# Optimization experiments

Measured on AMD Instinct MI355X. Metric: run time of the kernel, lower is better.

## Reference

```python
import jax, jax.numpy as jnp
import numpy as np

# OmniNet(deepqmc) reconstruction: ElectronicSchNet v1 (2 interactions, kernel_dim=8,
# embedding_dim=16, dist_feat_dim=4) + Linear(16,1,bias=False) orbital + sum over electrons.
# SchNet v1: shared w and g per interaction, spin-dependent h (same/anti), nuclear
# messages via learned nuclear embeddings Y. Subnets: w = 2-layer log-DNN 4->6->8 with SSP,
# h = Linear(16,8), g = Linear(8,16). SSP(x) = softplus(x) - log(2).

N_UP, N_DOWN = 16, 16
N_ELEC = N_UP + N_DOWN
N_ATOMS = 8
DIST_FEAT, KERNEL, EMBED = 4, 8, 16
N_INTER = 2
BATCH = 4096


def ssp(x):
    return jax.nn.softplus(x) - jnp.log(2.0).astype(x.dtype)


def setup_inputs() -> dict:
    key = jax.random.key(0)
    ks = jax.random.split(key, 16)
    s = 0.5  # init scale
    return {
        'dists_nuc': jax.random.uniform(ks[0], (BATCH, N_ELEC, N_ATOMS, DIST_FEAT), jnp.float32),
        'dists_elec': jax.random.uniform(ks[1], (BATCH, N_ELEC, N_ELEC, DIST_FEAT), jnp.float32),
        'X': jax.random.normal(ks[2], (1, EMBED), jnp.float32) * s,          # electron embedding (n_up==n_down)
        'Y': jax.random.normal(ks[3], (N_ATOMS, KERNEL), jnp.float32) * s,   # nuclear embeddings
        'w1': jax.random.normal(ks[4], (N_INTER, DIST_FEAT, 6), jnp.float32) * s,
        'wb1': jax.random.normal(ks[5], (N_INTER, 6), jnp.float32) * s,
        'w2': jax.random.normal(ks[6], (N_INTER, 6, KERNEL), jnp.float32) * s,
        'wb2': jax.random.normal(ks[7], (N_INTER, KERNEL), jnp.float32) * s,
        'hs_w': jax.random.normal(ks[8], (N_INTER, EMBED, KERNEL), jnp.float32) * s,
        'hs_b': jax.random.normal(ks[9], (N_INTER, KERNEL), jnp.float32) * s,
        'ha_w': jax.random.normal(ks[10], (N_INTER, EMBED, KERNEL), jnp.float32) * s,
        'ha_b': jax.random.normal(ks[11], (N_INTER, KERNEL), jnp.float32) * s,
        'g_w': jax.random.normal(ks[12], (N_INTER, KERNEL, EMBED), jnp.float32) * s,
        'g_b': jax.random.normal(ks[13], (N_INTER, EMBED), jnp.float32) * s,
        'orb_w': jax.random.normal(ks[14], (EMBED,), jnp.float32) * s,
    }


def reference(dists_nuc, dists_elec, X, Y, w1, wb1, w2, wb2, hs_w, hs_b, ha_w, ha_b, g_w, g_b, orb_w):
    B, n_elec = dists_elec.shape[:2]
    dt = dists_elec.dtype
    spins = jnp.concatenate([jnp.zeros(N_UP, jnp.int32), jnp.ones(N_DOWN, jnp.int32)])
    eye = jnp.eye(n_elec, dtype=bool)
    same = ((spins[:, None] == spins[None, :]) & ~eye).astype(dt)  # (i,j) same-spin, no self
    anti = (spins[:, None] != spins[None, :]).astype(dt)

    # initial embeddings: all electrons share X[0] since n_up == n_down
    x = jnp.broadcast_to(X[0], (B, n_elec, EMBED))

    for n in range(N_INTER):
        def w_net(e):  # (..., 4) -> (..., 8)
            return ssp(e @ w1[n] + wb1[n]) @ w2[n] + wb2[n]
        we = w_net(dists_elec)            # (B, i, j, K)
        wn = w_net(dists_nuc)             # (B, i, M, K)
        hs = x @ hs_w[n] + hs_b[n]        # (B, j, K) same-spin message features
        ha = x @ ha_w[n] + ha_b[n]        # (B, j, K) anti-spin
        z = (jnp.einsum('bijk,ij,bjk->bik', we, same, hs)
             + jnp.einsum('bijk,ij,bjk->bik', we, anti, ha)
             + jnp.einsum('bimk,mk->bik', wn, Y))
        x = x + (z @ g_w[n] + g_b[n])     # residual update

    # orbital projection (Linear(16,1,bias=False)), squeeze, sum over electrons
    return (x @ orb_w).sum(axis=-1)       # (B,)
```

## Files before the change

### kernel.cpp

```cpp
#include <hip/hip_runtime.h>

#define NE 32
#define NA 8
#define DF 4
#define KD 8
#define ED 16
#define BATCH 4096

#define WS_W1S0 0
#define WS_W1S1 24
#define WS_B1S0 48
#define WS_B1S1 54
#define WS_B2H0 60
#define WS_B2H1 68
#define WS_MS0  76
#define WS_MA0  84
#define WS_MS   92
#define WS_MA   156
#define WS_CS   220
#define WS_CA   228
#define WS_GO0  236
#define WS_GO1  244
#define WS_BASE 252

typedef float f32x2 __attribute__((ext_vector_type(2)));
__device__ __forceinline__ f32x2 splat2(float s) { f32x2 r; r.x = s; r.y = s; return r; }
__device__ __forceinline__ f32x2 fma2(f32x2 a, f32x2 b, f32x2 c) {
    return __builtin_elementwise_fma(a, b, c);
}

__global__ void omni_setup(const float* __restrict__ X,   const float* __restrict__ w1,
                           const float* __restrict__ wb1, const float* __restrict__ w2,
                           const float* __restrict__ wb2, const float* __restrict__ hs_w,
                           const float* __restrict__ hs_b,const float* __restrict__ ha_w,
                           const float* __restrict__ ha_b,const float* __restrict__ g_w,
                           const float* __restrict__ g_b, const float* __restrict__ orb_w,
                           float* __restrict__ ws)
{
    const int t = threadIdx.x;
    const float L   = 1.4426950408889634f;
    const float LN2 = 0.6931471805599453f;
    if (t < 48) {
        ws[t] = w1[t] * L;
    } else if (t < 60) {
        ws[t] = wb1[t - 48] * L;
    } else if (t < 76) {
        const int u = t - 60, n = u >> 3, k = u & 7;
        float sw = 0.f;
        for (int a = 0; a < 6; ++a) sw += w2[n * 48 + a * KD + k];
        ws[t] = wb2[n * KD + k] * L - sw;
    } else if (t < 92) {
        const int u = t - 76, tab = u >> 3, k = u & 7;
        const float* mw = tab ? ha_w : hs_w;
        const float* mb = tab ? ha_b : hs_b;
        float acc = mb[k];
        for (int c = 0; c < ED; ++c) acc += X[c] * mw[c * KD + k];
        ws[t] = acc;
    } else if (t < 220) {
        int u = t - 92; const int tab = u >> 6; u &= 63;
        const int kp = u >> 3, k = u & 7;
        const float* mw = (tab ? ha_w : hs_w) + ED * KD;
        float acc = 0.f;
        for (int c = 0; c < ED; ++c)
            acc += LN2 * g_w[kp * ED + c] * mw[c * KD + k];
        ws[t] = acc;
    } else if (t < 236) {
        const int u = t - 220, tab = u >> 3, k = u & 7;
        const float* mw = (tab ? ha_w : hs_w) + ED * KD;
        const float* mb = (tab ? ha_b : hs_b) + KD;
        float acc = mb[k];
        for (int c = 0; c < ED; ++c) acc += (X[c] + g_b[c]) * mw[c * KD + k];
        ws[t] = acc;
    } else if (t < 252) {
        const int u = t - 236, n = u >> 3, k = u & 7;
        float acc = 0.f;
        for (int c = 0; c < ED; ++c)
            acc += LN2 * g_w[n * KD * ED + k * ED + c] * orb_w[c];
        ws[t] = acc;
    } else if (t == 252) {
        float acc = 0.f;
        for (int c = 0; c < ED; ++c) acc += (X[c] + g_b[c] + g_b[ED + c]) * orb_w[c];
        ws[t] = acc;
    }
}

__device__ __forceinline__ void wnet_r2(const float4 e,
                                        const f32x2* __restrict__ vB1s2,
                                        const f32x2* __restrict__ sW12,
                                        f32x2* __restrict__ r2)
{
    #pragma unroll
    for (int a2 = 0; a2 < 3; ++a2) {
        f32x2 u = fma2(splat2(e.x), sW12[a2], vB1s2[a2]);
        u = fma2(splat2(e.y), sW12[3 + a2], u);
        u = fma2(splat2(e.z), sW12[6 + a2], u);
        u = fma2(splat2(e.w), sW12[9 + a2], u);
        f32x2 t;
        t.x = __builtin_amdgcn_exp2f(u.x);
        t.y = __builtin_amdgcn_exp2f(u.y);
        t = t + splat2(1.0f);
        r2[a2].x = __builtin_amdgcn_logf(t.x);
        r2[a2].y = __builtin_amdgcn_logf(t.y);
    }
}

__device__ __forceinline__ void proj2(const f32x2* __restrict__ r2,
                                      const f32x2* __restrict__ sW22,
                                      const f32x2* __restrict__ vB2h2,
                                      f32x2* __restrict__ racc2)
{
    #pragma unroll
    for (int k2 = 0; k2 < 4; ++k2) {
        f32x2 acc = vB2h2[k2];
        acc = fma2(splat2(r2[0].x), sW22[0 * 4 + k2], acc);
        acc = fma2(splat2(r2[0].y), sW22[1 * 4 + k2], acc);
        acc = fma2(splat2(r2[1].x), sW22[2 * 4 + k2], acc);
        acc = fma2(splat2(r2[1].y), sW22[3 * 4 + k2], acc);
        acc = fma2(splat2(r2[2].x), sW22[4 * 4 + k2], acc);
        acc = fma2(splat2(r2[2].y), sW22[5 * 4 + k2], acc);
        racc2[k2] = acc;
    }
}

__global__ __launch_bounds__(256) void omni_main(
    const float* __restrict__ dists_nuc,
    const float* __restrict__ dists_elec,
    const float* __restrict__ Y,
    const float* __restrict__ w2,
    const float* __restrict__ ws,
    float* __restrict__ out)
{
    const int tid  = threadIdx.x;
    const int w    = tid >> 6;
    const int lane = tid & 63;
    const int ie   = lane & 7;
    const int joct = lane >> 3;
    const int ig   = 8 * w + ie;
    const int b    = blockIdx.x;
    const int h    = ig >> 4;
    const int sj   = joct >> 2;
    const bool same = (sj == h);
    const int t32  = same ? 0 : 32;

    __shared__ float4 ebuf[4 * 256];
    __shared__ float msg[65][KD];
    __shared__ float part[4];
    if (tid < KD) msg[64][tid] = 0.0f;

    const f32x2* ws2  = (const f32x2*)ws;
    const f32x2* w2p0 = (const f32x2*)w2;
    const f32x2* w2p1 = (const f32x2*)(w2 + 48);
    const f32x2* Yp   = (const f32x2*)Y;

    const float* de = dists_elec + (((size_t)b * NE + ig) * NE + 4 * joct) * DF;
    const float* dn = dists_nuc  + (((size_t)b * NE + ig) * NA + joct) * DF;
    const float4* de4 = (const float4*)de;

    const float4 nr0 = *(const float4*)dn;

    float zr0[KD];
    {
        f32x2 vB1s2[3], vB2h2[4], msel2[4];
        #pragma unroll
        for (int a2 = 0; a2 < 3; ++a2) vB1s2[a2] = ws2[WS_B1S0 / 2 + a2];
        #pragma unroll
        for (int k2 = 0; k2 < 4; ++k2) vB2h2[k2] = ws2[WS_B2H0 / 2 + k2];
        #pragma unroll
        for (int k2 = 0; k2 < 4; ++k2)
            msel2[k2] = same ? ws2[WS_MS0 / 2 + k2] : ws2[WS_MA0 / 2 + k2];

        const int scnt  = ig - 4 * joct;
        const float fcnt = (joct == (ig >> 2)) ? 3.0f : 4.0f;
        f32x2 S2[3] = {splat2(0.f), splat2(0.f), splat2(0.f)};
        #pragma unroll
        for (int s = 0; s < 4; ++s) {
            const float4 e = de4[s];
            ebuf[s * 256 + tid] = e;
            f32x2 r2[3];
            wnet_r2(e, vB1s2, ws2 + WS_W1S0 / 2, r2);
            const float mf = (s == scnt) ? 0.0f : 1.0f;
            #pragma unroll
            for (int a2 = 0; a2 < 3; ++a2) S2[a2] = fma2(r2[a2], splat2(mf), S2[a2]);
        }
        f32x2 z2[4];
        #pragma unroll
        for (int k2 = 0; k2 < 4; ++k2) {
            f32x2 acc = splat2(fcnt) * vB2h2[k2];
            acc = fma2(splat2(S2[0].x), w2p0[0 * 4 + k2], acc);
            acc = fma2(splat2(S2[0].y), w2p0[1 * 4 + k2], acc);
            acc = fma2(splat2(S2[1].x), w2p0[2 * 4 + k2], acc);
            acc = fma2(splat2(S2[1].y), w2p0[3 * 4 + k2], acc);
            acc = fma2(splat2(S2[2].x), w2p0[4 * 4 + k2], acc);
            acc = fma2(splat2(S2[2].y), w2p0[5 * 4 + k2], acc);
            z2[k2] = acc * msel2[k2];
        }
        {
            f32x2 r2[3], racc2[4];
            wnet_r2(nr0, vB1s2, ws2 + WS_W1S0 / 2, r2);
            proj2(r2, w2p0, vB2h2, racc2);
            #pragma unroll
            for (int k2 = 0; k2 < 4; ++k2)
                z2[k2] = fma2(racc2[k2], Yp[joct * 4 + k2], z2[k2]);
        }
        #pragma unroll
        for (int k2 = 0; k2 < 4; ++k2) {
            float za = z2[k2].x, zb = z2[k2].y;
            za += __shfl_xor(za, 8, 64); za += __shfl_xor(za, 16, 64); za += __shfl_xor(za, 32, 64);
            zb += __shfl_xor(zb, 8, 64); zb += __shfl_xor(zb, 16, 64); zb += __shfl_xor(zb, 32, 64);
            zr0[2 * k2] = za; zr0[2 * k2 + 1] = zb;
        }
    }

    {
        f32x2 ms2[4], ma2[4];
        #pragma unroll
        for (int k2 = 0; k2 < 4; ++k2) {
            ms2[k2] = ws2[WS_CS / 2 + k2];
            ma2[k2] = ws2[WS_CA / 2 + k2];
        }
        #pragma unroll
        for (int kp = 0; kp < KD; ++kp) {
            const f32x2 zk = splat2(zr0[kp]);
            #pragma unroll
            for (int k2 = 0; k2 < 4; ++k2) {
                ms2[k2] = fma2(zk, ws2[WS_MS / 2 + kp * 4 + k2], ms2[k2]);
                ma2[k2] = fma2(zk, ws2[WS_MA / 2 + kp * 4 + k2], ma2[k2]);
            }
        }
        if (joct == 0) {
            #pragma unroll
            for (int k2 = 0; k2 < 4; ++k2) *(f32x2*)&msg[ig][2 * k2] = ms2[k2];
        } else if (joct == 4) {
            #pragma unroll
            for (int k2 = 0; k2 < 4; ++k2) *(f32x2*)&msg[32 + ig][2 * k2] = ma2[k2];
        }
    }

    float dot = ws[WS_BASE];
    #pragma unroll
    for (int k = 0; k < KD; ++k) dot = fmaf(zr0[k], ws[WS_GO0 + k], dot);

    __syncthreads();

    float zr1[KD];
    {
        f32x2 vB1s2[3], vB2h2[4];
        #pragma unroll
        for (int a2 = 0; a2 < 3; ++a2) vB1s2[a2] = ws2[WS_B1S1 / 2 + a2];
        #pragma unroll
        for (int k2 = 0; k2 < 4; ++k2) vB2h2[k2] = ws2[WS_B2H1 / 2 + k2];

        f32x2 z2[4] = {splat2(0.f), splat2(0.f), splat2(0.f), splat2(0.f)};
        #pragma unroll
        for (int s = 0; s < 4; ++s) {
            const float4 e = ebuf[s * 256 + tid];
            f32x2 r2[3], racc2[4];
            wnet_r2(e, vB1s2, ws2 + WS_W1S1 / 2, r2);
            proj2(r2, w2p1, vB2h2, racc2);
            const int j = 4 * joct + s;
            const int row = (j == ig) ? 64 : (t32 + j);
            const f32x2* mrow = (const f32x2*)&msg[row][0];
            #pragma unroll
            for (int k2 = 0; k2 < 4; ++k2) z2[k2] = fma2(racc2[k2], mrow[k2], z2[k2]);
        }
        {
            f32x2 r2[3], racc2[4];
            wnet_r2(nr0, vB1s2, ws2 + WS_W1S1 / 2, r2);
            proj2(r2, w2p1, vB2h2, racc2);
            #pragma unroll
            for (int k2 = 0; k2 < 4; ++k2)
                z2[k2] = fma2(racc2[k2], Yp[joct * 4 + k2], z2[k2]);
        }
        #pragma unroll
        for (int k2 = 0; k2 < 4; ++k2) {
            float za = z2[k2].x, zb = z2[k2].y;
            za += __shfl_xor(za, 8, 64); za += __shfl_xor(za, 16, 64); za += __shfl_xor(za, 32, 64);
            zb += __shfl_xor(zb, 8, 64); zb += __shfl_xor(zb, 16, 64); zb += __shfl_xor(zb, 32, 64);
            zr1[2 * k2] = za; zr1[2 * k2 + 1] = zb;
        }
    }

    #pragma unroll
    for (int k = 0; k < KD; ++k) dot = fmaf(zr1[k], ws[WS_GO1 + k], dot);
    dot *= 0.125f;
    #pragma unroll
    for (int off = 1; off < 64; off <<= 1) dot += __shfl_xor(dot, off, 64);
    if (lane == 0) part[w] = dot;
    __syncthreads();
    if (tid == 0) out[b] = part[0] + part[1] + part[2] + part[3];
}

extern "C" void kernel_launch(void* const* d_in, const int* in_sizes, int n_in,
                              void* d_out, int out_size, void* d_ws, size_t ws_size,
                              hipStream_t stream) {
    const float* dists_nuc  = (const float*)d_in[0];
    const float* dists_elec = (const float*)d_in[1];
    const float* X     = (const float*)d_in[2];
    const float* Y     = (const float*)d_in[3];
    const float* w1    = (const float*)d_in[4];
    const float* wb1   = (const float*)d_in[5];
    const float* w2    = (const float*)d_in[6];
    const float* wb2   = (const float*)d_in[7];
    const float* hs_w  = (const float*)d_in[8];
    const float* hs_b  = (const float*)d_in[9];
    const float* ha_w  = (const float*)d_in[10];
    const float* ha_b  = (const float*)d_in[11];
    const float* g_w   = (const float*)d_in[12];
    const float* g_b   = (const float*)d_in[13];
    const float* orb_w = (const float*)d_in[14];
    float* out = (float*)d_out;
    float* ws  = (float*)d_ws;

    omni_setup<<<1, 256, 0, stream>>>(X, w1, wb1, w2, wb2, hs_w, hs_b,
                                      ha_w, ha_b, g_w, g_b, orb_w, ws);
    omni_main<<<BATCH, 256, 0, stream>>>(dists_nuc, dists_elec, Y, w2, ws, out);
}
```

Measured before the change: 146.0 us.

## Process two batch samples per block with register prefetch of the next sample

```diff
diff --git a/kernel.cpp b/kernel.cpp
--- a/kernel.cpp
+++ b/kernel.cpp
@@ -136,7 +136,6 @@
     const int ie   = lane & 7;
     const int joct = lane >> 3;
     const int ig   = 8 * w + ie;
-    const int b    = blockIdx.x;
     const int h    = ig >> 4;
     const int sj   = joct >> 2;
     const bool same = (sj == h);
@@ -152,142 +151,162 @@
     const f32x2* w2p1 = (const f32x2*)(w2 + 48);
     const f32x2* Yp   = (const f32x2*)Y;
 
-    const float* de = dists_elec + (((size_t)b * NE + ig) * NE + 4 * joct) * DF;
-    const float* dn = dists_nuc  + (((size_t)b * NE + ig) * NA + joct) * DF;
-    const float4* de4 = (const float4*)de;
-
-    const float4 nr0 = *(const float4*)dn;
-
-    float zr0[KD];
+    const int b0 = 2 * blockIdx.x;
+    const size_t deS = (size_t)NE * NE * DF;
+    const size_t dnS = (size_t)NE * NA * DF;
+    const float* de = dists_elec + (((size_t)b0 * NE + ig) * NE + 4 * joct) * DF;
+    const float* dn = dists_nuc  + (((size_t)b0 * NE + ig) * NA + joct) * DF;
+
+    float4 pe[4];
     {
-        f32x2 vB1s2[3], vB2h2[4], msel2[4];
+        const float4* p = (const float4*)de;
         #pragma unroll
-        for (int a2 = 0; a2 < 3; ++a2) vB1s2[a2] = ws2[WS_B1S0 / 2 + a2];
+        for (int s = 0; s < 4; ++s) pe[s] = p[s];
+    }
+    float4 pn = *(const float4*)dn;
+    float4 qn;
+
+    f32x2 vB1s0[3], vB1s1[3], vB2h0[4], vB2h1[4], msel2[4];
+    #pragma unroll
+    for (int a2 = 0; a2 < 3; ++a2) {
+        vB1s0[a2] = ws2[WS_B1S0 / 2 + a2];
+        vB1s1[a2] = ws2[WS_B1S1 / 2 + a2];
+    }
+    #pragma unroll
+    for (int k2 = 0; k2 < 4; ++k2) {
+        vB2h0[k2] = ws2[WS_B2H0 / 2 + k2];
+        vB2h1[k2] = ws2[WS_B2H1 / 2 + k2];
+        msel2[k2] = same ? ws2[WS_MS0 / 2 + k2] : ws2[WS_MA0 / 2 + k2];
+    }
+    const int scnt   = ig - 4 * joct;
+    const float fcnt = (joct == (ig >> 2)) ? 3.0f : 4.0f;
+
+    #pragma unroll
+    for (int smp = 0; smp < 2; ++smp) {
+        float zr0[KD];
+        {
+            f32x2 S2[3] = {splat2(0.f), splat2(0.f), splat2(0.f)};
+            #pragma unroll
+            for (int s = 0; s < 4; ++s) {
+                const float4 e = pe[s];
+                ebuf[s * 256 + tid] = e;
+                f32x2 r2[3];
+                wnet_r2(e, vB1s0, ws2 + WS_W1S0 / 2, r2);
+                const float mf = (s == scnt) ? 0.0f : 1.0f;
+                #pragma unroll
+                for (int a2 = 0; a2 < 3; ++a2) S2[a2] = fma2(r2[a2], splat2(mf), S2[a2]);
+            }
+
+            if (smp == 0) {
+                const float4* p = (const float4*)(de + deS);
+                #pragma unroll
+                for (int s = 0; s < 4; ++s) pe[s] = p[s];
+                qn = *(const float4*)(dn + dnS);
+            }
+
+            f32x2 z2[4];
+            #pragma unroll
+            for (int k2 = 0; k2 < 4; ++k2) {
+                f32x2 acc = splat2(fcnt) * vB2h0[k2];
+                acc = fma2(splat2(S2[0].x), w2p0[0 * 4 + k2], acc);
+                acc = fma2(splat2(S2[0].y), w2p0[1 * 4 + k2], acc);
+                acc = fma2(splat2(S2[1].x), w2p0[2 * 4 + k2], acc);
+                acc = fma2(splat2(S2[1].y), w2p0[3 * 4 + k2], acc);
+                acc = fma2(splat2(S2[2].x), w2p0[4 * 4 + k2], acc);
+                acc = fma2(splat2(S2[2].y), w2p0[5 * 4 + k2], acc);
+                z2[k2] = acc * msel2[k2];
+            }
+            {
+                f32x2 r2[3], racc2[4];
+                wnet_r2(pn, vB1s0, ws2 + WS_W1S0 / 2, r2);
+                proj2(r2, w2p0, vB2h0, racc2);
+                #pragma unroll
+                for (int k2 = 0; k2 < 4; ++k2)
+                    z2[k2] = fma2(racc2[k2], Yp[joct * 4 + k2], z2[k2]);
+            }
+            #pragma unroll
+            for (int k2 = 0; k2 < 4; ++k2) {
+                float za = z2[k2].x, zb = z2[k2].y;
+                za += __shfl_xor(za, 8, 64); za += __shfl_xor(za, 16, 64); za += __shfl_xor(za, 32, 64);
+                zb += __shfl_xor(zb, 8, 64); zb += __shfl_xor(zb, 16, 64); zb += __shfl_xor(zb, 32, 64);
+                zr0[2 * k2] = za; zr0[2 * k2 + 1] = zb;
+            }
+        }
+
+        {
+            f32x2 ms2[4], ma2[4];
+            #pragma unroll
+            for (int k2 = 0; k2 < 4; ++k2) {
+                ms2[k2] = ws2[WS_CS / 2 + k2];
+                ma2[k2] = ws2[WS_CA / 2 + k2];
+            }
+            #pragma unroll
+            for (int kp = 0; kp < KD; ++kp) {
+                const f32x2 zk = splat2(zr0[kp]);
+                #pragma unroll
+                for (int k2 = 0; k2 < 4; ++k2) {
+                    ms2[k2] = fma2(zk, ws2[WS_MS / 2 + kp * 4 + k2], ms2[k2]);
+                    ma2[k2] = fma2(zk, ws2[WS_MA / 2 + kp * 4 + k2], ma2[k2]);
+                }
+            }
+            if (joct == 0) {
+                #pragma unroll
+                for (int k2 = 0; k2 < 4; ++k2) *(f32x2*)&msg[ig][2 * k2] = ms2[k2];
+            } else if (joct == 4) {
+                #pragma unroll
+                for (int k2 = 0; k2 < 4; ++k2) *(f32x2*)&msg[32 + ig][2 * k2] = ma2[k2];
+            }
+        }
+
+        float dot = ws[WS_BASE];
         #pragma unroll
-        for (int k2 = 0; k2 < 4; ++k2) vB2h2[k2] = ws2[WS_B2H0 / 2 + k2];
+        for (int k = 0; k < KD; ++k) dot = fmaf(zr0[k], ws[WS_GO0 + k], dot);
+
+        __syncthreads();
+
+        float zr1[KD];
+        {
+            f32x2 z2[4] = {splat2(0.f), splat2(0.f), splat2(0.f), splat2(0.f)};
+            #pragma unroll
+            for (int s = 0; s < 4; ++s) {
+                const float4 e = ebuf[s * 256 + tid];
+                f32x2 r2[3], racc2[4];
+                wnet_r2(e, vB1s1, ws2 + WS_W1S1 / 2, r2);
+                proj2(r2, w2p1, vB2h1, racc2);
+                const int j = 4 * joct + s;
+                const int row = (j == ig) ? 64 : (t32 + j);
+                const f32x2* mrow = (const f32x2*)&msg[row][0];
+                #pragma unroll
+                for (int k2 = 0; k2 < 4; ++k2) z2[k2] = fma2(racc2[k2], mrow[k2], z2[k2]);
+            }
+            {
+                f32x2 r2[3], racc2[4];
+                wnet_r2(pn, vB1s1, ws2 + WS_W1S1 / 2, r2);
+                proj2(r2, w2p1, vB2h1, racc2);
+                #pragma unroll
+                for (int k2 = 0; k2 < 4; ++k2)
+                    z2[k2] = fma2(racc2[k2], Yp[joct * 4 + k2], z2[k2]);
+            }
+            #pragma unroll
+            for (int k2 = 0; k2 < 4; ++k2) {
+                float za = z2[k2].x, zb = z2[k2].y;
+                za += __shfl_xor(za, 8, 64); za += __shfl_xor(za, 16, 64); za += __shfl_xor(za, 32, 64);
+                zb += __shfl_xor(zb, 8, 64); zb += __shfl_xor(zb, 16, 64); zb += __shfl_xor(zb, 32, 64);
+                zr1[2 * k2] = za; zr1[2 * k2 + 1] = zb;
+            }
+        }
+
         #pragma unroll
-        for (int k2 = 0; k2 < 4; ++k2)
-            msel2[k2] = same ? ws2[WS_MS0 / 2 + k2] : ws2[WS_MA0 / 2 + k2];
-
-        const int scnt  = ig - 4 * joct;
-        const float fcnt = (joct == (ig >> 2)) ? 3.0f : 4.0f;
-        f32x2 S2[3] = {splat2(0.f), splat2(0.f), splat2(0.f)};
+        for (int k = 0; k < KD; ++k) dot = fmaf(zr1[k], ws[WS_GO1 + k], dot);
+        dot *= 0.125f;
         #pragma unroll
-        for (int s = 0; s < 4; ++s) {
-            const float4 e = de4[s];
-            ebuf[s * 256 + tid] = e;
-            f32x2 r2[3];
-            wnet_r2(e, vB1s2, ws2 + WS_W1S0 / 2, r2);
-            const float mf = (s == scnt) ? 0.0f : 1.0f;
-            #pragma unroll
-            for (int a2 = 0; a2 < 3; ++a2) S2[a2] = fma2(r2[a2], splat2(mf), S2[a2]);
-        }
-        f32x2 z2[4];
-        #pragma unroll
-        for (int k2 = 0; k2 < 4; ++k2) {
-            f32x2 acc = splat2(fcnt) * vB2h2[k2];
-            acc = fma2(splat2(S2[0].x), w2p0[0 * 4 + k2], acc);
-            acc = fma2(splat2(S2[0].y), w2p0[1 * 4 + k2], acc);
-            acc = fma2(splat2(S2[1].x), w2p0[2 * 4 + k2], acc);
-            acc = fma2(splat2(S2[1].y), w2p0[3 * 4 + k2], acc);
-            acc = fma2(splat2(S2[2].x), w2p0[4 * 4 + k2], acc);
-            acc = fma2(splat2(S2[2].y), w2p0[5 * 4 + k2], acc);
-            z2[k2] = acc * msel2[k2];
-        }
-        {
-            f32x2 r2[3], racc2[4];
-            wnet_r2(nr0, vB1s2, ws2 + WS_W1S0 / 2, r2);
-            proj2(r2, w2p0, vB2h2, racc2);
-            #pragma unroll
-            for (int k2 = 0; k2 < 4; ++k2)
-                z2[k2] = fma2(racc2[k2], Yp[joct * 4 + k2], z2[k2]);
-        }
-        #pragma unroll
-        for (int k2 = 0; k2 < 4; ++k2) {
-            float za = z2[k2].x, zb = z2[k2].y;
-            za += __shfl_xor(za, 8, 64); za += __shfl_xor(za, 16, 64); za += __shfl_xor(za, 32, 64);
-            zb += __shfl_xor(zb, 8, 64); zb += __shfl_xor(zb, 16, 64); zb += __shfl_xor(zb, 32, 64);
-            zr0[2 * k2] = za; zr0[2 * k2 + 1] = zb;
-        }
-    }
-
-    {
-        f32x2 ms2[4], ma2[4];
-        #pragma unroll
-        for (int k2 = 0; k2 < 4; ++k2) {
-            ms2[k2] = ws2[WS_CS / 2 + k2];
-            ma2[k2] = ws2[WS_CA / 2 + k2];
-        }
-        #pragma unroll
-        for (int kp = 0; kp < KD; ++kp) {
-            const f32x2 zk = splat2(zr0[kp]);
-            #pragma unroll
-            for (int k2 = 0; k2 < 4; ++k2) {
-                ms2[k2] = fma2(zk, ws2[WS_MS / 2 + kp * 4 + k2], ms2[k2]);
-                ma2[k2] = fma2(zk, ws2[WS_MA / 2 + kp * 4 + k2], ma2[k2]);
-            }
-        }
-        if (joct == 0) {
-            #pragma unroll
-            for (int k2 = 0; k2 < 4; ++k2) *(f32x2*)&msg[ig][2 * k2] = ms2[k2];
-        } else if (joct == 4) {
-            #pragma unroll
-            for (int k2 = 0; k2 < 4; ++k2) *(f32x2*)&msg[32 + ig][2 * k2] = ma2[k2];
-        }
-    }
-
-    float dot = ws[WS_BASE];
-    #pragma unroll
-    for (int k = 0; k < KD; ++k) dot = fmaf(zr0[k], ws[WS_GO0 + k], dot);
-
-    __syncthreads();
-
-    float zr1[KD];
-    {
-        f32x2 vB1s2[3], vB2h2[4];
-        #pragma unroll
-        for (int a2 = 0; a2 < 3; ++a2) vB1s2[a2] = ws2[WS_B1S1 / 2 + a2];
-        #pragma unroll
-        for (int k2 = 0; k2 < 4; ++k2) vB2h2[k2] = ws2[WS_B2H1 / 2 + k2];
-
-        f32x2 z2[4] = {splat2(0.f), splat2(0.f), splat2(0.f), splat2(0.f)};
-        #pragma unroll
-        for (int s = 0; s < 4; ++s) {
-            const float4 e = ebuf[s * 256 + tid];
-            f32x2 r2[3], racc2[4];
-            wnet_r2(e, vB1s2, ws2 + WS_W1S1 / 2, r2);
-            proj2(r2, w2p1, vB2h2, racc2);
-            const int j = 4 * joct + s;
-            const int row = (j == ig) ? 64 : (t32 + j);
-            const f32x2* mrow = (const f32x2*)&msg[row][0];
-            #pragma unroll
-            for (int k2 = 0; k2 < 4; ++k2) z2[k2] = fma2(racc2[k2], mrow[k2], z2[k2]);
-        }
-        {
-            f32x2 r2[3], racc2[4];
-            wnet_r2(nr0, vB1s2, ws2 + WS_W1S1 / 2, r2);
-            proj2(r2, w2p1, vB2h2, racc2);
-            #pragma unroll
-            for (int k2 = 0; k2 < 4; ++k2)
-                z2[k2] = fma2(racc2[k2], Yp[joct * 4 + k2], z2[k2]);
-        }
-        #pragma unroll
-        for (int k2 = 0; k2 < 4; ++k2) {
-            float za = z2[k2].x, zb = z2[k2].y;
-            za += __shfl_xor(za, 8, 64); za += __shfl_xor(za, 16, 64); za += __shfl_xor(za, 32, 64);
-            zb += __shfl_xor(zb, 8, 64); zb += __shfl_xor(zb, 16, 64); zb += __shfl_xor(zb, 32, 64);
-            zr1[2 * k2] = za; zr1[2 * k2 + 1] = zb;
-        }
-    }
-
-    #pragma unroll
-    for (int k = 0; k < KD; ++k) dot = fmaf(zr1[k], ws[WS_GO1 + k], dot);
-    dot *= 0.125f;
-    #pragma unroll
-    for (int off = 1; off < 64; off <<= 1) dot += __shfl_xor(dot, off, 64);
-    if (lane == 0) part[w] = dot;
-    __syncthreads();
-    if (tid == 0) out[b] = part[0] + part[1] + part[2] + part[3];
+        for (int off = 1; off < 64; off <<= 1) dot += __shfl_xor(dot, off, 64);
+        if (lane == 0) part[w] = dot;
+        __syncthreads();
+        if (tid == 0) out[b0 + smp] = part[0] + part[1] + part[2] + part[3];
+
+        if (smp == 0) pn = qn;
+    }
 }
 
 extern "C" void kernel_launch(void* const* d_in, const int* in_sizes, int n_in,
@@ -313,5 +332,5 @@
 
     omni_setup<<<1, 256, 0, stream>>>(X, w1, wb1, w2, wb2, hs_w, hs_b,
                                       ha_w, ha_b, g_w, g_b, orb_w, ws);
-    omni_main<<<BATCH, 256, 0, stream>>>(dists_nuc, dists_elec, Y, w2, ws, out);
-}
+    omni_main<<<BATCH / 2, 256, 0, stream>>>(dists_nuc, dists_elec, Y, w2, ws, out);
+}
```

Result: no change. 145.8 us (-0.1%).
